# Kernel optimization log

Hardware: AMD Instinct MI355X
Metric: run time of the kernel (lower is better)

Reference implementation:

```python
import jax, jax.numpy as jnp
import numpy as np

B, T, D_MODEL, N_HEAD, D_C = 2, 2048, 2048, 16, 512
D_HEAD = D_MODEL // N_HEAD          # 128
D_ROPE = D_C // N_HEAD              # 32 (rope projections are split into heads too)


def setup_inputs() -> dict:
    key = jax.random.key(0)
    ks = jax.random.split(key, 16)
    s = 0.02
    # weights stored as [in, out] (transpose of torch Linear.weight)
    return {
        "x":     jax.random.normal(ks[0], (B, T, D_MODEL), jnp.float32),
        "W_DKV": jax.random.normal(ks[1], (D_MODEL, D_C), jnp.float32) * s,
        "b_DKV": jnp.zeros((D_C,), jnp.float32),
        "W_UK":  jax.random.normal(ks[2], (D_C, D_MODEL), jnp.float32) * s,
        "b_UK":  jnp.zeros((D_MODEL,), jnp.float32),
        "W_UV":  jax.random.normal(ks[3], (D_C, D_MODEL), jnp.float32) * s,
        "b_UV":  jnp.zeros((D_MODEL,), jnp.float32),
        "W_DQ":  jax.random.normal(ks[4], (D_MODEL, D_C), jnp.float32) * s,
        "b_DQ":  jnp.zeros((D_C,), jnp.float32),
        "W_UQ":  jax.random.normal(ks[5], (D_C, D_MODEL), jnp.float32) * s,
        "b_UQ":  jnp.zeros((D_MODEL,), jnp.float32),
        "W_QR":  jax.random.normal(ks[6], (D_C, D_C), jnp.float32) * s,
        "b_QR":  jnp.zeros((D_C,), jnp.float32),
        "W_KR":  jax.random.normal(ks[7], (D_MODEL, D_C), jnp.float32) * s,
        "b_KR":  jnp.zeros((D_C,), jnp.float32),
    }


def _rope(x):
    # x: [B, H, T, d]; matches torch RoPE: split-even/odd then concat halves
    t, d = x.shape[2], x.shape[-1]
    freqs = 10000.0 ** (-(jnp.arange(0, d, 2, dtype=jnp.float32) / d))  # [d/2]
    theta = jnp.arange(t, dtype=jnp.float32)[:, None] * freqs[None, :]  # [T, d/2]
    cos, sin = jnp.cos(theta), jnp.sin(theta)
    x1, x2 = x[..., ::2], x[..., 1::2]
    return jnp.concatenate([x1 * cos - x2 * sin, x1 * sin + x2 * cos], axis=-1)


def _heads(x):
    b, t, _ = x.shape
    return x.reshape(b, t, N_HEAD, -1).transpose(0, 2, 1, 3)  # [B,H,T,dh]


def reference(x, W_DKV, b_DKV, W_UK, b_UK, W_UV, b_UV, W_DQ, b_DQ,
              W_UQ, b_UQ, W_QR, b_QR, W_KR, b_KR):
    b, t, _ = x.shape
    c_kv = x @ W_DKV + b_DKV                 # [B,T,d_c]
    k_content = _heads(c_kv @ W_UK + b_UK)   # [B,H,T,d_head]
    v = _heads(c_kv @ W_UV + b_UV)           # [B,H,T,d_head]
    c_q = x @ W_DQ + b_DQ
    q_content = _heads(c_q @ W_UQ + b_UQ)    # [B,H,T,d_head]
    q_rope = _rope(_heads(c_q @ W_QR + b_QR))  # [B,H,T,d_rope]
    k_rope = _rope(_heads(x @ W_KR + b_KR))    # [B,H,T,d_rope]
    Q = jnp.concatenate([q_content, q_rope], axis=-1)  # [B,H,T,d_head+d_rope]
    K = jnp.concatenate([k_content, k_rope], axis=-1)
    scale = 1.0 / jnp.sqrt(jnp.float32(Q.shape[-1]))
    scores = jnp.einsum("bhqd,bhkd->bhqk", Q, K) * scale
    probs = jax.nn.softmax(scores, axis=-1)
    out = jnp.einsum("bhqk,bhkd->bhqd", probs, v)
    return out.transpose(0, 2, 1, 3).reshape(b, t, -1)
```

## Files before the change

kernel.cpp:

```cpp
#include <hip/hip_runtime.h>
#include <hip/hip_bf16.h>
#include <cstdint>
#include <cstddef>

typedef __attribute__((ext_vector_type(8)))  short bf16x8;
typedef __attribute__((ext_vector_type(4)))  float f32x4;
typedef __attribute__((ext_vector_type(16))) float f32x16;
typedef __attribute__((ext_vector_type(4)))  int   i32x4;

#define DEVINL __device__ __forceinline__

#define QSCALE (0.07905694150420949f * 1.4426950408889634f)

DEVINL unsigned short f2bf(float f) {
  unsigned int u = __float_as_uint(f);
  u += 0x7fff + ((u >> 16) & 1);
  return (unsigned short)(u >> 16);
}

DEVINL int cvtpk(float lo, float hi) {
  int r;
  asm("v_cvt_pk_bf16_f32 %0, %1, %2" : "=v"(r) : "v"(lo), "v"(hi));
  return r;
}

DEVINL void stage16(const unsigned short* __restrict__ g, unsigned short* lds_u) {
  __builtin_amdgcn_global_load_lds((const __attribute__((address_space(1))) void*)g,
                                   (__attribute__((address_space(3))) void*)lds_u, 16, 0, 0);
}

struct TwArgs { const float* W[7]; unsigned short* D[7]; };
__global__ void k_prep(const float* __restrict__ x, unsigned short* __restrict__ xb, TwArgs a) {
  __shared__ float t[32][33];
  const int bid = blockIdx.x, tid = threadIdx.x;
  if (bid < 8192) {
    const int i = (bid * 256 + tid) * 4;
    float4 v = *reinterpret_cast<const float4*>(x + i);
    ushort4 r;
    r.x = f2bf(v.x); r.y = f2bf(v.y); r.z = f2bf(v.z); r.w = f2bf(v.w);
    *reinterpret_cast<ushort4*>(xb + i) = r;
    return;
  }
  const int tb = bid - 8192;
  int w, K, N, bx, by;
  if (tb < 3072)      { w = tb >> 10; int r = tb & 1023; K = 2048; N = 512;  bx = r & 15; by = r >> 4; }
  else if (tb < 6144) { int r = tb - 3072; w = 3 + (r >> 10); r &= 1023; K = 512; N = 2048; bx = r & 63; by = r >> 6; }
  else                 { int r = tb - 6144; w = 6; K = 512; N = 512; bx = r & 15; by = r >> 4; }
  const float* W = a.W[w];
  unsigned short* D = a.D[w];
  const int n0 = bx * 32, k0 = by * 32;
  const int tx = tid & 31, ty = tid >> 5;
#pragma unroll
  for (int j = 0; j < 4; j++)
    t[ty + j * 8][tx] = W[(size_t)(k0 + ty + j * 8) * N + n0 + tx];
  __syncthreads();
#pragma unroll
  for (int j = 0; j < 4; j++)
    D[(size_t)(n0 + ty + j * 8) * K + k0 + tx] = f2bf(t[tx][ty + j * 8]);
}

DEVINL size_t koff(int bh, int t, int d) {
  const int it = t >> 6, t6 = t & 63;
  const int kvt = t6 >> 5, lanelo = t6 & 31;
  const int ks = d >> 4, hi = (d >> 3) & 1, e = d & 7;
  return ((size_t)bh * 32 + it) * 10240 + (size_t)(kvt * 10 + ks) * 512 + (hi * 32 + lanelo) * 8 + e;
}
DEVINL size_t voff(int bh, int t, int dv) {
  const int it = t >> 6, t6 = t & 63;
  const int ks = t6 >> 4, hi = (t6 >> 3) & 1, e = t6 & 7;
  const int dvt = dv >> 5, lanelo = dv & 31;
  return ((size_t)bh * 32 + it) * 8192 + (size_t)(dvt * 4 + ks) * 512 + (hi * 32 + lanelo) * 8 + e;
}

__global__ __launch_bounds__(256) void k_gemm1(const unsigned short* __restrict__ A,
                                               const unsigned short* __restrict__ BT,
                                               const float* __restrict__ bias0,
                                               const float* __restrict__ bias1,
                                               const float* __restrict__ bias2,
                                               unsigned short* __restrict__ o0,
                                               unsigned short* __restrict__ o1,
                                               float* __restrict__ o2) {
  __shared__ unsigned short sA[128 * 64];
  __shared__ unsigned short sB[64 * 64];
  const int K = 2048;
  const int tid = threadIdx.x;
  const int lane = tid & 63, wid = tid >> 6;
  const int row0 = blockIdx.y * 128, col0 = blockIdx.x * 64;
  const int lc = lane & 15, lg = lane >> 4;
  const int srow = lane >> 3, scol = (lane & 7) * 8;

  f32x4 acc[2][4];
#pragma unroll
  for (int m = 0; m < 2; m++)
#pragma unroll
    for (int n = 0; n < 4; n++) acc[m][n] = f32x4{0.f, 0.f, 0.f, 0.f};

  for (int k0 = 0; k0 < K; k0 += 64) {
#pragma unroll
    for (int i = 0; i < 6; i++) {
      const int chunk = wid * 6 + i;
      if (chunk < 16) {
        stage16(A + (size_t)(row0 + chunk * 8 + srow) * K + k0 + scol, sA + chunk * 512);
      } else {
        const int c = chunk - 16;
        stage16(BT + (size_t)(col0 + c * 8 + srow) * K + k0 + scol, sB + c * 512);
      }
    }
    asm volatile("s_waitcnt vmcnt(0)" ::: "memory");
    __syncthreads();
#pragma unroll
    for (int ks = 0; ks < 2; ks++) {
      bf16x8 af[2], bfr[4];
#pragma unroll
      for (int m = 0; m < 2; m++)
        af[m] = *reinterpret_cast<const bf16x8*>(sA + (wid * 32 + m * 16 + lc) * 64 + ks * 32 + lg * 8);
#pragma unroll
      for (int n = 0; n < 4; n++)
        bfr[n] = *reinterpret_cast<const bf16x8*>(sB + (n * 16 + lc) * 64 + ks * 32 + lg * 8);
#pragma unroll
      for (int m = 0; m < 2; m++)
#pragma unroll
        for (int n = 0; n < 4; n++)
          acc[m][n] = __builtin_amdgcn_mfma_f32_16x16x32_bf16(af[m], bfr[n], acc[m][n], 0, 0, 0);
    }
    __syncthreads();
  }

  const int seg = col0 >> 9;
  const int cofs = col0 - seg * 512;
  const float* bp = (seg == 0) ? bias0 : (seg == 1) ? bias1 : bias2;
  const int lr = lg * 4;
#pragma unroll
  for (int m = 0; m < 2; m++)
#pragma unroll
    for (int n = 0; n < 4; n++) {
      const int c = cofs + n * 16 + lc;
      const float bv = bp[c];
#pragma unroll
      for (int r = 0; r < 4; r++) {
        const int row = row0 + wid * 32 + m * 16 + lr + r;
        const float v = acc[m][n][r] + bv;
        if (seg == 0)      o0[(size_t)row * 512 + c] = f2bf(v);
        else if (seg == 1) o1[(size_t)row * 512 + c] = f2bf(v);
        else               o2[(size_t)row * 512 + c] = v;
      }
    }
}

__global__ __launch_bounds__(256) void k_gemm2(const unsigned short* __restrict__ ckv,
                                               const unsigned short* __restrict__ cq,
                                               const unsigned short* __restrict__ WT2,
                                               const unsigned short* __restrict__ WT3,
                                               const float* __restrict__ bUK,
                                               const float* __restrict__ bUV,
                                               const float* __restrict__ bUQ,
                                               const float* __restrict__ bQR,
                                               unsigned short* __restrict__ Kfb,
                                               unsigned short* __restrict__ Vfb,
                                               unsigned short* __restrict__ Qbuf,
                                               float* __restrict__ qrp) {
  __shared__ unsigned short sA[128 * 64];
  __shared__ unsigned short sB[128 * 64];
  const int K = 512;
  const int bx = blockIdx.x;
  const bool m11 = bx < 32;
  const unsigned short* A  = m11 ? ckv : cq;
  const unsigned short* BT = m11 ? WT2 : WT3;
  const int tid = threadIdx.x;
  const int lane = tid & 63, wid = tid >> 6;
  const int wr = wid >> 1, wc = wid & 1;
  const int row0 = blockIdx.y * 128;
  const int col0 = (m11 ? bx : (bx - 32)) * 128;
  const int lc = lane & 15, lg = lane >> 4;
  const int srow = lane >> 3, scol = (lane & 7) * 8;

  f32x4 acc[4][4];
#pragma unroll
  for (int m = 0; m < 4; m++)
#pragma unroll
    for (int n = 0; n < 4; n++) acc[m][n] = f32x4{0.f, 0.f, 0.f, 0.f};

  for (int k0 = 0; k0 < K; k0 += 64) {
#pragma unroll
    for (int i = 0; i < 4; i++) {
      const int chunk = wid * 4 + i;
      const int r = chunk * 8 + srow;
      stage16(A + (size_t)(row0 + r) * K + k0 + scol, sA + chunk * 512);
      stage16(BT + (size_t)(col0 + r) * K + k0 + scol, sB + chunk * 512);
    }
    asm volatile("s_waitcnt vmcnt(0)" ::: "memory");
    __syncthreads();
#pragma unroll
    for (int ks = 0; ks < 2; ks++) {
      bf16x8 af[4], bfr[4];
#pragma unroll
      for (int m = 0; m < 4; m++)
        af[m] = *reinterpret_cast<const bf16x8*>(sA + (wr * 64 + m * 16 + lc) * 64 + ks * 32 + lg * 8);
#pragma unroll
      for (int n = 0; n < 4; n++)
        bfr[n] = *reinterpret_cast<const bf16x8*>(sB + (wc * 64 + n * 16 + lc) * 64 + ks * 32 + lg * 8);
#pragma unroll
      for (int m = 0; m < 4; m++)
#pragma unroll
        for (int n = 0; n < 4; n++)
          acc[m][n] = __builtin_amdgcn_mfma_f32_16x16x32_bf16(af[m], bfr[n], acc[m][n], 0, 0, 0);
    }
    __syncthreads();
  }

  const int lr = lg * 4;
  const int b = blockIdx.y >> 4;
  const int t0 = (blockIdx.y & 15) * 128;

  if (bx < 16) {
    const int bh = b * 16 + bx;
#pragma unroll
    for (int m = 0; m < 4; m++)
#pragma unroll
      for (int n = 0; n < 4; n++) {
        const int d = wc * 64 + n * 16 + lc;
        const float bv = bUK[bx * 128 + d];
        const int t = t0 + wr * 64 + m * 16 + lr;
        const size_t ko = koff(bh, t, d);
#pragma unroll
        for (int r = 0; r < 4; r++)
          Kfb[ko + 8 * r] = f2bf(acc[m][n][r] + bv);
      }
  } else if (bx < 32) {
    const int h = bx - 16, bh = b * 16 + h;
#pragma unroll
    for (int m = 0; m < 4; m++)
#pragma unroll
      for (int n = 0; n < 4; n++) {
        const int dv = wc * 64 + n * 16 + lc;
        const float bv = bUV[h * 128 + dv];
        const int t = t0 + wr * 64 + m * 16 + lr;
        const size_t vo = voff(bh, t, dv);
        ushort4 pk;
        pk.x = f2bf(acc[m][n][0] + bv);
        pk.y = f2bf(acc[m][n][1] + bv);
        pk.z = f2bf(acc[m][n][2] + bv);
        pk.w = f2bf(acc[m][n][3] + bv);
        *reinterpret_cast<ushort4*>(Vfb + vo) = pk;
      }
  } else if (bx < 48) {
    const int h = bx - 32;
#pragma unroll
    for (int m = 0; m < 4; m++)
#pragma unroll
      for (int n = 0; n < 4; n++) {
        const int d = wc * 64 + n * 16 + lc;
        const float bv = bUQ[h * 128 + d];
        const int t = t0 + wr * 64 + m * 16 + lr;
        size_t qo = ((size_t)(b * 16 + h) * 2048 + t) * 160 + d;
#pragma unroll
        for (int r = 0; r < 4; r++) {
          Qbuf[qo] = f2bf((acc[m][n][r] + bv) * QSCALE);
          qo += 160;
        }
      }
  } else {
    const int c0 = (bx - 48) * 128;
#pragma unroll
    for (int m = 0; m < 4; m++)
#pragma unroll
      for (int n = 0; n < 4; n++) {
        const int c = c0 + wc * 64 + n * 16 + lc;
        const float bv = bQR[c];
#pragma unroll
        for (int r = 0; r < 4; r++) {
          const int row = blockIdx.y * 128 + wr * 64 + m * 16 + lr + r;
          qrp[(size_t)row * 512 + c] = acc[m][n][r] + bv;
        }
      }
  }
}

__global__ void k_rope(const float* __restrict__ qpre, const float* __restrict__ kpre,
                       unsigned short* __restrict__ Qb, unsigned short* __restrict__ Kf) {
  const int idx = blockIdx.x * blockDim.x + threadIdx.x;
  const int which = idx >> 20;
  const int e = idx & 1048575;
  const int i = e & 15, h = (e >> 4) & 15, row = e >> 8;
  const int t = row & 2047, b = row >> 11;
  const float* pre = which ? kpre : qpre;
  const float x1 = pre[(size_t)row * 512 + h * 32 + 2 * i];
  const float x2 = pre[(size_t)row * 512 + h * 32 + 2 * i + 1];
  const float f = exp2f(-(float)i * (13.287712379549449f / 16.f));
  const float th = (float)t * f;
  float sv, cv;
  sincosf(th, &sv, &cv);
  const float o1 = x1 * cv - x2 * sv, o2 = x1 * sv + x2 * cv;
  if (which == 0) {
    const size_t base = ((size_t)(b * 16 + h) * 2048 + t) * 160 + 128;
    Qb[base + i]      = f2bf(o1 * QSCALE);
    Qb[base + 16 + i] = f2bf(o2 * QSCALE);
  } else {
    Kf[koff(b * 16 + h, t, 128 + i)] = f2bf(o1);
    Kf[koff(b * 16 + h, t, 144 + i)] = f2bf(o2);
  }
}

__global__ __launch_bounds__(256, 2) void k_attn(const unsigned short* __restrict__ Qb,
                                                 const unsigned short* __restrict__ Kf,
                                                 const unsigned short* __restrict__ Vf,
                                                 float* __restrict__ out) {
  __shared__ unsigned short sK[2][10240];
  const int lane = threadIdx.x & 63, wid = threadIdx.x >> 6;
  const int lanelo = lane & 31, hi = lane >> 5;

  const int L = blockIdx.x;
  const int xcd = L & 7, w = L >> 3;
  const int bh = xcd * 4 + (w & 3);
  const int qblk = w >> 2;
  const int b = bh >> 4, h = bh & 15;
  const int q0 = qblk * 128 + wid * 32;

  const unsigned short* Qh = Qb + (size_t)bh * 2048 * 160;
  const unsigned short* Kh = Kf + (size_t)bh * 32 * 10240;
  const unsigned short* Vh = Vf + (size_t)bh * 32 * 8192;

  bf16x8 qf[10];
#pragma unroll
  for (int ks = 0; ks < 10; ks++)
    qf[ks] = *reinterpret_cast<const bf16x8*>(Qh + (size_t)(q0 + lanelo) * 160 + ks * 16 + hi * 8);

#pragma unroll
  for (int i = 0; i < 5; i++) {
    const int chunk = wid * 5 + i;
    stage16(Kh + (size_t)chunk * 512 + lane * 8, &sK[0][0] + chunk * 512);
  }

  f32x16 o[4] = {};
  float mrun = -1e30f, lrun = 0.f;

  asm volatile("s_waitcnt vmcnt(0)" ::: "memory");
  __syncthreads();

  int buf = 0;
  for (int it = 0; it < 32; it++) {
    bf16x8 vf[16];
    {
      const unsigned short* Vt = Vh + (size_t)it * 8192;
#pragma unroll
      for (int f = 0; f < 16; f++)
        vf[f] = *reinterpret_cast<const bf16x8*>(Vt + (size_t)f * 512 + lane * 8);
    }
    if (it < 31) {
      const unsigned short* src = Kh + (size_t)(it + 1) * 10240;
      unsigned short* dst = &sK[buf ^ 1][0];
#pragma unroll
      for (int i = 0; i < 5; i++) {
        const int chunk = wid * 5 + i;
        stage16(src + (size_t)chunk * 512 + lane * 8, dst + chunk * 512);
      }
    }
    f32x16 s0 = {}, s1 = {};
    const unsigned short* sKb = &sK[buf][0];
#pragma unroll
    for (int ks = 0; ks < 10; ks++) {
      bf16x8 kf0 = *reinterpret_cast<const bf16x8*>(sKb + (size_t)ks * 512 + lane * 8);
      s0 = __builtin_amdgcn_mfma_f32_32x32x16_bf16(kf0, qf[ks], s0, 0, 0, 0);
      bf16x8 kf1 = *reinterpret_cast<const bf16x8*>(sKb + (size_t)(10 + ks) * 512 + lane * 8);
      s1 = __builtin_amdgcn_mfma_f32_32x32x16_bf16(kf1, qf[ks], s1, 0, 0, 0);
    }

    float tm[16];
#pragma unroll
    for (int j = 0; j < 16; j++) tm[j] = fmaxf(s0[j], s1[j]);
#pragma unroll
    for (int s = 8; s >= 1; s >>= 1)
#pragma unroll
      for (int j = 0; j < s; j++) tm[j] = fmaxf(tm[j], tm[j + s]);
    float mx = fmaxf(tm[0], __shfl_xor(tm[0], 32));

    if (__any(mx > mrun + 8.f)) {
      const float mn = fmaxf(mrun, mx);
      const float corr = exp2f(mrun - mn);
      lrun *= corr;
#pragma unroll
      for (int d = 0; d < 4; d++)
#pragma unroll
        for (int r = 0; r < 16; r++) o[d][r] *= corr;
      mrun = mn;
    }

    float pe0[16], pe1[16];
#pragma unroll
    for (int r = 0; r < 16; r++) pe0[r] = exp2f(s0[r] - mrun);
#pragma unroll
    for (int r = 0; r < 16; r++) pe1[r] = exp2f(s1[r] - mrun);
    float ta[16];
#pragma unroll
    for (int j = 0; j < 8; j++) {
      ta[j]     = pe0[2 * j] + pe0[2 * j + 1];
      ta[8 + j] = pe1[2 * j] + pe1[2 * j + 1];
    }
#pragma unroll
    for (int s = 8; s >= 1; s >>= 1)
#pragma unroll
      for (int j = 0; j < s; j++) ta[j] += ta[j + s];
    lrun += ta[0] + __shfl_xor(ta[0], 32);

    int W0[8], W1[8], S0w[8], S1w[8];
#pragma unroll
    for (int j = 0; j < 8; j++) {
      W0[j] = cvtpk(pe0[2 * j], pe0[2 * j + 1]);
      W1[j] = cvtpk(pe1[2 * j], pe1[2 * j + 1]);
    }
#pragma unroll
    for (int j = 0; j < 8; j++) {
      S0w[j] = __shfl_xor(W0[j], 32);
      S1w[j] = __shfl_xor(W1[j], 32);
    }
    bf16x8 pa[4];
    {
      i32x4 w0 = hi ? i32x4{S0w[2], S0w[3], W0[2], W0[3]} : i32x4{W0[0], W0[1], S0w[0], S0w[1]};
      i32x4 w1 = hi ? i32x4{S0w[6], S0w[7], W0[6], W0[7]} : i32x4{W0[4], W0[5], S0w[4], S0w[5]};
      i32x4 w2 = hi ? i32x4{S1w[2], S1w[3], W1[2], W1[3]} : i32x4{W1[0], W1[1], S1w[0], S1w[1]};
      i32x4 w3 = hi ? i32x4{S1w[6], S1w[7], W1[6], W1[7]} : i32x4{W1[4], W1[5], S1w[4], S1w[5]};
      pa[0] = __builtin_bit_cast(bf16x8, w0);
      pa[1] = __builtin_bit_cast(bf16x8, w1);
      pa[2] = __builtin_bit_cast(bf16x8, w2);
      pa[3] = __builtin_bit_cast(bf16x8, w3);
    }

#pragma unroll
    for (int ks = 0; ks < 4; ks++) {
      o[0] = __builtin_amdgcn_mfma_f32_32x32x16_bf16(vf[ks],      pa[ks], o[0], 0, 0, 0);
      o[1] = __builtin_amdgcn_mfma_f32_32x32x16_bf16(vf[4 + ks],  pa[ks], o[1], 0, 0, 0);
      o[2] = __builtin_amdgcn_mfma_f32_32x32x16_bf16(vf[8 + ks],  pa[ks], o[2], 0, 0, 0);
      o[3] = __builtin_amdgcn_mfma_f32_32x32x16_bf16(vf[12 + ks], pa[ks], o[3], 0, 0, 0);
    }

    asm volatile("s_waitcnt vmcnt(0)" ::: "memory");
    __syncthreads();
    buf ^= 1;
  }

  const float inv = 1.f / lrun;
  float* sO = reinterpret_cast<float*>(&sK[0][0]) + wid * 1152;
#pragma unroll
  for (int dvt = 0; dvt < 4; dvt++) {
    __syncthreads();
#pragma unroll
    for (int r = 0; r < 16; r++) {
      const int dvl = (r & 3) + 8 * (r >> 2) + 4 * hi;
      sO[lanelo * 36 + dvl] = o[dvt][r] * inv;
    }
    __syncthreads();
#pragma unroll
    for (int p = 0; p < 4; p++) {
      const int q = p * 8 + (lane >> 3), c = (lane & 7) * 4;
      float4 v = *reinterpret_cast<const float4*>(sO + q * 36 + c);
      *reinterpret_cast<float4*>(out + ((size_t)b * 2048 + q0 + q) * 2048 + h * 128 + dvt * 32 + c) = v;
    }
  }
}

extern "C" void kernel_launch(void* const* d_in, const int* in_sizes, int n_in,
                              void* d_out, int out_size, void* d_ws, size_t ws_size,
                              hipStream_t stream) {
  (void)in_sizes; (void)n_in; (void)out_size;
  const float* x     = (const float*)d_in[0];
  const float* W_DKV = (const float*)d_in[1];
  const float* b_DKV = (const float*)d_in[2];
  const float* W_UK  = (const float*)d_in[3];
  const float* b_UK  = (const float*)d_in[4];
  const float* W_UV  = (const float*)d_in[5];
  const float* b_UV  = (const float*)d_in[6];
  const float* W_DQ  = (const float*)d_in[7];
  const float* b_DQ  = (const float*)d_in[8];
  const float* W_UQ  = (const float*)d_in[9];
  const float* b_UQ  = (const float*)d_in[10];
  const float* W_QR  = (const float*)d_in[11];
  const float* b_QR  = (const float*)d_in[12];
  const float* W_KR  = (const float*)d_in[13];
  const float* b_KR  = (const float*)d_in[14];
  float* out = (float*)d_out;

  char* ws = (char*)d_ws;
  unsigned short* xb     = (unsigned short*)(ws + 0);
  unsigned short* WTcat1 = (unsigned short*)(ws + 16777216);
  unsigned short* WTcat2 = (unsigned short*)(ws + 23068672);
  unsigned short* WTcat3 = (unsigned short*)(ws + 27262976);
  unsigned short* ckv    = (unsigned short*)(ws + 29884416);
  unsigned short* cq     = (unsigned short*)(ws + 34078720);
  unsigned short* Qbuf   = (unsigned short*)(ws + 38273024);
  unsigned short* Kfb    = (unsigned short*)(ws + 59244544);
  unsigned short* Vfb    = (unsigned short*)(ws + 80216064);
  float*          qrp    = (float*)(ws + 96993280);
  float*          krp    = (float*)(ws + 105381888);
  if (ws_size < 113770496) return;

  TwArgs ta;
  ta.W[0] = W_DKV; ta.D[0] = WTcat1;
  ta.W[1] = W_DQ;  ta.D[1] = WTcat1 + (size_t)512 * 2048;
  ta.W[2] = W_KR;  ta.D[2] = WTcat1 + (size_t)1024 * 2048;
  ta.W[3] = W_UK;  ta.D[3] = WTcat2;
  ta.W[4] = W_UV;  ta.D[4] = WTcat2 + (size_t)2048 * 512;
  ta.W[5] = W_UQ;  ta.D[5] = WTcat3;
  ta.W[6] = W_QR;  ta.D[6] = WTcat3 + (size_t)2048 * 512;
  k_prep<<<14592, 256, 0, stream>>>(x, xb, ta);

  k_gemm1<<<dim3(24, 32), 256, 0, stream>>>(xb, WTcat1, b_DKV, b_DQ, b_KR, ckv, cq, krp);
  k_gemm2<<<dim3(52, 32), 256, 0, stream>>>(ckv, cq, WTcat2, WTcat3,
                                            b_UK, b_UV, b_UQ, b_QR,
                                            Kfb, Vfb, Qbuf, qrp);

  k_rope<<<8192, 256, 0, stream>>>(qrp, krp, Qbuf, Kfb);
  k_attn<<<512, 256, 0, stream>>>(Qbuf, Kfb, Vfb, out);
}
```

Baseline: 340.4 us.

## Fuse RoPE into GEMM epilogues and split attention KV across two wave groups

Applies RoPE directly in the gemm1 and gemm2 epilogues, using a lane shuffle to pair even and odd elements. This removes the separate rope kernel and its fp32 intermediate buffers. The attention kernel now runs 512 threads per block, with two groups of four waves each handling half of the KV sequence (flash-decoding style split). The two partial softmax states are then merged through LDS. The goal is more parallelism and latency hiding in attention, at the cost of doubled LDS, an extra merge step, and sincos work inside the GEMM epilogues.

```diff
diff --git a/kernel.cpp b/kernel.cpp
--- a/kernel.cpp
+++ b/kernel.cpp
@@ -11,6 +11,7 @@
 #define DEVINL __device__ __forceinline__
 
 #define QSCALE (0.07905694150420949f * 1.4426950408889634f)
+#define RFREQ  0.830482023721841f
 
 DEVINL unsigned short f2bf(float f) {
   unsigned int u = __float_as_uint(f);
@@ -79,7 +80,7 @@
                                                const float* __restrict__ bias2,
                                                unsigned short* __restrict__ o0,
                                                unsigned short* __restrict__ o1,
-                                               float* __restrict__ o2) {
+                                               unsigned short* __restrict__ Kfb) {
   __shared__ unsigned short sA[128 * 64];
   __shared__ unsigned short sB[64 * 64];
   const int K = 2048;
@@ -130,21 +131,46 @@
   const int cofs = col0 - seg * 512;
   const float* bp = (seg == 0) ? bias0 : (seg == 1) ? bias1 : bias2;
   const int lr = lg * 4;
-#pragma unroll
-  for (int m = 0; m < 2; m++)
-#pragma unroll
-    for (int n = 0; n < 4; n++) {
-      const int c = cofs + n * 16 + lc;
-      const float bv = bp[c];
-#pragma unroll
-      for (int r = 0; r < 4; r++) {
-        const int row = row0 + wid * 32 + m * 16 + lr + r;
-        const float v = acc[m][n][r] + bv;
-        if (seg == 0)      o0[(size_t)row * 512 + c] = f2bf(v);
-        else if (seg == 1) o1[(size_t)row * 512 + c] = f2bf(v);
-        else               o2[(size_t)row * 512 + c] = v;
-      }
-    }
+
+  if (seg < 2) {
+#pragma unroll
+    for (int m = 0; m < 2; m++)
+#pragma unroll
+      for (int n = 0; n < 4; n++) {
+        const int c = cofs + n * 16 + lc;
+        const float bv = bp[c];
+#pragma unroll
+        for (int r = 0; r < 4; r++) {
+          const int row = row0 + wid * 32 + m * 16 + lr + r;
+          const float v = acc[m][n][r] + bv;
+          if (seg == 0) o0[(size_t)row * 512 + c] = f2bf(v);
+          else          o1[(size_t)row * 512 + c] = f2bf(v);
+        }
+      }
+  } else {
+    const int par = lane & 1;
+#pragma unroll
+    for (int m = 0; m < 2; m++)
+#pragma unroll
+      for (int n = 0; n < 4; n++) {
+        const int c = cofs + n * 16 + lc;
+        const float bv = bp[c];
+        const int i = (c & 31) >> 1, hh = c >> 5;
+        const float freq = exp2f(-(float)i * RFREQ);
+        const int d = 128 + (par << 4) + i;
+#pragma unroll
+        for (int r = 0; r < 4; r++) {
+          const int row = row0 + wid * 32 + m * 16 + lr + r;
+          const int t = row & 2047, bb = row >> 11;
+          const float v = acc[m][n][r] + bv;
+          const float vp = __shfl_xor(v, 1);
+          float sv, cv;
+          sincosf((float)t * freq, &sv, &cv);
+          const float ov = par ? (vp * sv + v * cv) : (v * cv - vp * sv);
+          Kfb[koff(bb * 16 + hh, t, d)] = f2bf(ov);
+        }
+      }
+  }
 }
 
 __global__ __launch_bounds__(256) void k_gemm2(const unsigned short* __restrict__ ckv,
@@ -157,8 +183,7 @@
                                                const float* __restrict__ bQR,
                                                unsigned short* __restrict__ Kfb,
                                                unsigned short* __restrict__ Vfb,
-                                               unsigned short* __restrict__ Qbuf,
-                                               float* __restrict__ qrp) {
+                                               unsigned short* __restrict__ Qbuf) {
   __shared__ unsigned short sA[128 * 64];
   __shared__ unsigned short sB[128 * 64];
   const int K = 512;
@@ -261,52 +286,39 @@
       }
   } else {
     const int c0 = (bx - 48) * 128;
+    const int par = lane & 1;
 #pragma unroll
     for (int m = 0; m < 4; m++)
 #pragma unroll
       for (int n = 0; n < 4; n++) {
         const int c = c0 + wc * 64 + n * 16 + lc;
         const float bv = bQR[c];
+        const int i = (c & 31) >> 1, hh = c >> 5;
+        const float freq = exp2f(-(float)i * RFREQ);
+        const int d = 128 + (par << 4) + i;
 #pragma unroll
         for (int r = 0; r < 4; r++) {
           const int row = blockIdx.y * 128 + wr * 64 + m * 16 + lr + r;
-          qrp[(size_t)row * 512 + c] = acc[m][n][r] + bv;
+          const int t = row & 2047, bb = row >> 11;
+          const float v = acc[m][n][r] + bv;
+          const float vp = __shfl_xor(v, 1);
+          float sv, cv;
+          sincosf((float)t * freq, &sv, &cv);
+          const float ov = par ? (vp * sv + v * cv) : (v * cv - vp * sv);
+          Qbuf[((size_t)(bb * 16 + hh) * 2048 + t) * 160 + d] = f2bf(ov * QSCALE);
         }
       }
   }
 }
 
-__global__ void k_rope(const float* __restrict__ qpre, const float* __restrict__ kpre,
-                       unsigned short* __restrict__ Qb, unsigned short* __restrict__ Kf) {
-  const int idx = blockIdx.x * blockDim.x + threadIdx.x;
-  const int which = idx >> 20;
-  const int e = idx & 1048575;
-  const int i = e & 15, h = (e >> 4) & 15, row = e >> 8;
-  const int t = row & 2047, b = row >> 11;
-  const float* pre = which ? kpre : qpre;
-  const float x1 = pre[(size_t)row * 512 + h * 32 + 2 * i];
-  const float x2 = pre[(size_t)row * 512 + h * 32 + 2 * i + 1];
-  const float f = exp2f(-(float)i * (13.287712379549449f / 16.f));
-  const float th = (float)t * f;
-  float sv, cv;
-  sincosf(th, &sv, &cv);
-  const float o1 = x1 * cv - x2 * sv, o2 = x1 * sv + x2 * cv;
-  if (which == 0) {
-    const size_t base = ((size_t)(b * 16 + h) * 2048 + t) * 160 + 128;
-    Qb[base + i]      = f2bf(o1 * QSCALE);
-    Qb[base + 16 + i] = f2bf(o2 * QSCALE);
-  } else {
-    Kf[koff(b * 16 + h, t, 128 + i)] = f2bf(o1);
-    Kf[koff(b * 16 + h, t, 144 + i)] = f2bf(o2);
-  }
-}
-
-__global__ __launch_bounds__(256, 2) void k_attn(const unsigned short* __restrict__ Qb,
+__global__ __launch_bounds__(512, 4) void k_attn(const unsigned short* __restrict__ Qb,
                                                  const unsigned short* __restrict__ Kf,
                                                  const unsigned short* __restrict__ Vf,
                                                  float* __restrict__ out) {
-  __shared__ unsigned short sK[2][10240];
-  const int lane = threadIdx.x & 63, wid = threadIdx.x >> 6;
+  __shared__ unsigned short sK[2][2][10240];
+  const int tid = threadIdx.x;
+  const int lane = tid & 63, wid = tid >> 6;
+  const int qw = wid & 3, kvh = wid >> 2;
   const int lanelo = lane & 31, hi = lane >> 5;
 
   const int L = blockIdx.x;
@@ -314,11 +326,11 @@
   const int bh = xcd * 4 + (w & 3);
   const int qblk = w >> 2;
   const int b = bh >> 4, h = bh & 15;
-  const int q0 = qblk * 128 + wid * 32;
+  const int q0 = qblk * 128 + qw * 32;
 
   const unsigned short* Qh = Qb + (size_t)bh * 2048 * 160;
-  const unsigned short* Kh = Kf + (size_t)bh * 32 * 10240;
-  const unsigned short* Vh = Vf + (size_t)bh * 32 * 8192;
+  const unsigned short* Kh = Kf + ((size_t)bh * 32 + kvh * 16) * 10240;
+  const unsigned short* Vh = Vf + ((size_t)bh * 32 + kvh * 16) * 8192;
 
   bf16x8 qf[10];
 #pragma unroll
@@ -327,8 +339,8 @@
 
 #pragma unroll
   for (int i = 0; i < 5; i++) {
-    const int chunk = wid * 5 + i;
-    stage16(Kh + (size_t)chunk * 512 + lane * 8, &sK[0][0] + chunk * 512);
+    const int chunk = qw * 5 + i;
+    stage16(Kh + (size_t)chunk * 512 + lane * 8, &sK[kvh][0][0] + chunk * 512);
   }
 
   f32x16 o[4] = {};
@@ -338,7 +350,7 @@
   __syncthreads();
 
   int buf = 0;
-  for (int it = 0; it < 32; it++) {
+  for (int it = 0; it < 16; it++) {
     bf16x8 vf[16];
     {
       const unsigned short* Vt = Vh + (size_t)it * 8192;
@@ -346,17 +358,17 @@
       for (int f = 0; f < 16; f++)
         vf[f] = *reinterpret_cast<const bf16x8*>(Vt + (size_t)f * 512 + lane * 8);
     }
-    if (it < 31) {
+    if (it < 15) {
       const unsigned short* src = Kh + (size_t)(it + 1) * 10240;
-      unsigned short* dst = &sK[buf ^ 1][0];
+      unsigned short* dst = &sK[kvh][buf ^ 1][0];
 #pragma unroll
       for (int i = 0; i < 5; i++) {
-        const int chunk = wid * 5 + i;
+        const int chunk = qw * 5 + i;
         stage16(src + (size_t)chunk * 512 + lane * 8, dst + chunk * 512);
       }
     }
     f32x16 s0 = {}, s1 = {};
-    const unsigned short* sKb = &sK[buf][0];
+    const unsigned short* sKb = &sK[kvh][buf][0];
 #pragma unroll
     for (int ks = 0; ks < 10; ks++) {
       bf16x8 kf0 = *reinterpret_cast<const bf16x8*>(sKb + (size_t)ks * 512 + lane * 8);
@@ -438,22 +450,55 @@
     buf ^= 1;
   }
 
+  float* scr = reinterpret_cast<float*>(&sK[0][0][0]);
+  if (kvh == 1) {
+    float* p = scr + (size_t)(qw * 32 + lanelo) * 130;
+#pragma unroll
+    for (int dvt = 0; dvt < 4; dvt++)
+#pragma unroll
+      for (int r = 0; r < 16; r++) {
+        const int dvl = (r & 3) + 8 * (r >> 2) + 4 * hi;
+        p[dvt * 32 + dvl] = o[dvt][r];
+      }
+    if (hi == 0) { p[128] = mrun; p[129] = lrun; }
+  }
+  __syncthreads();
+  if (kvh == 0) {
+    const float* p = scr + (size_t)(qw * 32 + lanelo) * 130;
+    const float mB = p[128], lB = p[129];
+    const float M = fmaxf(mrun, mB);
+    const float aA = exp2f(mrun - M), aB = exp2f(mB - M);
+    lrun = aA * lrun + aB * lB;
+#pragma unroll
+    for (int dvt = 0; dvt < 4; dvt++)
+#pragma unroll
+      for (int r = 0; r < 16; r++) {
+        const int dvl = (r & 3) + 8 * (r >> 2) + 4 * hi;
+        o[dvt][r] = aA * o[dvt][r] + aB * p[dvt * 32 + dvl];
+      }
+  }
+  __syncthreads();
+
   const float inv = 1.f / lrun;
-  float* sO = reinterpret_cast<float*>(&sK[0][0]) + wid * 1152;
+  float* sO = scr + wid * 1152;
 #pragma unroll
   for (int dvt = 0; dvt < 4; dvt++) {
     __syncthreads();
-#pragma unroll
-    for (int r = 0; r < 16; r++) {
-      const int dvl = (r & 3) + 8 * (r >> 2) + 4 * hi;
-      sO[lanelo * 36 + dvl] = o[dvt][r] * inv;
-    }
-    __syncthreads();
-#pragma unroll
-    for (int p = 0; p < 4; p++) {
-      const int q = p * 8 + (lane >> 3), c = (lane & 7) * 4;
-      float4 v = *reinterpret_cast<const float4*>(sO + q * 36 + c);
-      *reinterpret_cast<float4*>(out + ((size_t)b * 2048 + q0 + q) * 2048 + h * 128 + dvt * 32 + c) = v;
+    if (kvh == 0) {
+#pragma unroll
+      for (int r = 0; r < 16; r++) {
+        const int dvl = (r & 3) + 8 * (r >> 2) + 4 * hi;
+        sO[lanelo * 36 + dvl] = o[dvt][r] * inv;
+      }
+    }
+    __syncthreads();
+    if (kvh == 0) {
+#pragma unroll
+      for (int p = 0; p < 4; p++) {
+        const int q = p * 8 + (lane >> 3), c = (lane & 7) * 4;
+        float4 v = *reinterpret_cast<const float4*>(sO + q * 36 + c);
+        *reinterpret_cast<float4*>(out + ((size_t)b * 2048 + q0 + q) * 2048 + h * 128 + dvt * 32 + c) = v;
+      }
     }
   }
 }
@@ -489,9 +534,7 @@
   unsigned short* Qbuf   = (unsigned short*)(ws + 38273024);
   unsigned short* Kfb    = (unsigned short*)(ws + 59244544);
   unsigned short* Vfb    = (unsigned short*)(ws + 80216064);
-  float*          qrp    = (float*)(ws + 96993280);
-  float*          krp    = (float*)(ws + 105381888);
-  if (ws_size < 113770496) return;
+  if (ws_size < 96993280) return;
 
   TwArgs ta;
   ta.W[0] = W_DKV; ta.D[0] = WTcat1;
@@ -503,11 +546,10 @@
   ta.W[6] = W_QR;  ta.D[6] = WTcat3 + (size_t)2048 * 512;
   k_prep<<<14592, 256, 0, stream>>>(x, xb, ta);
 
-  k_gemm1<<<dim3(24, 32), 256, 0, stream>>>(xb, WTcat1, b_DKV, b_DQ, b_KR, ckv, cq, krp);
+  k_gemm1<<<dim3(24, 32), 256, 0, stream>>>(xb, WTcat1, b_DKV, b_DQ, b_KR, ckv, cq, Kfb);
   k_gemm2<<<dim3(52, 32), 256, 0, stream>>>(ckv, cq, WTcat2, WTcat3,
                                             b_UK, b_UV, b_UQ, b_QR,
-                                            Kfb, Vfb, Qbuf, qrp);
-
-  k_rope<<<8192, 256, 0, stream>>>(qrp, krp, Qbuf, Kfb);
-  k_attn<<<512, 256, 0, stream>>>(Qbuf, Kfb, Vfb, out);
-}
+                                            Kfb, Vfb, Qbuf);
+
+  k_attn<<<512, 512, 0, stream>>>(Qbuf, Kfb, Vfb, out);
+}
```

New measurement: 906.1 us. 166% more time.
